# Performance work log

Measured on AMD Instinct MI355X. Metric: run time of the kernel, lower is better.

## Reference

```python
import jax, jax.numpy as jnp
import numpy as np


def setup_inputs() -> dict:
    key = jax.random.key(0)
    k1, k2 = jax.random.split(key)
    x = jax.random.normal(k1, (8, 4096, 256), dtype=jnp.float32)
    embed = jax.random.normal(k2, (1, 8192, 256), dtype=jnp.float32)
    return {"x": x, "embed": embed}


def reference(x, embed):
    # EuclideanCodebook.forward, eval mode, sample_codebook_temp=0.
    # x: [b, n, d]  (ndim < 4 -> a leading codebook dim h=1 is added)
    # embed: [h, c, d]
    xf = x.astype(jnp.float32)[None]              # [h, b, n, d]
    h, b, n, d = xf.shape
    flatten = xf.reshape(h, b * n, d)             # [h, N, d]

    # dist = -cdist(flatten, embed, p=2)
    x2 = jnp.sum(flatten * flatten, axis=-1, keepdims=True)   # [h, N, 1]
    e2 = jnp.sum(embed * embed, axis=-1)                      # [h, c]
    xe = jnp.einsum('hnd,hcd->hnc', flatten, embed)           # [h, N, c]
    d2 = jnp.maximum(x2 + e2[:, None, :] - 2.0 * xe, 0.0)
    dist = -jnp.sqrt(d2)                                      # [h, N, c]

    # gumbel_sample with temperature == 0  ->  argmax
    embed_ind = jnp.argmax(dist, axis=-1)                     # [h, N]
    embed_ind = embed_ind.reshape(h, b, n)                    # [h, b, n]

    # batched_embedding: gather codes per codebook
    quantize = jax.vmap(lambda e, i: e[i])(embed, embed_ind)  # [h, b, n, d]

    # needs_codebook_dim -> squeeze leading h
    return quantize[0], embed_ind[0]
```

## Files before the change

kernel.cpp:

```cpp
#include <hip/hip_runtime.h>
#include <math.h>

#define D       256
#define NROWS   32768
#define CODES   8192
#define QOFF    8388608

#define BM      128
#define BN      128
#define NSPL    4
#define SPLC    (CODES / NSPL)
#define NCHUNK  (SPLC / BN)
#define NSTEP   (NCHUNK * 4)
#define NBLK    1024
#define LQ      2048

#define MARG_COEF 0.016f
#define MARG_ABS  0.10f

#define OFF_AH    0ull
#define OFF_X2    16777216ull
#define OFF_NX    16908288ull
#define OFF_E2    17039360ull
#define OFF_RM    17072128ull
#define OFF_PK    17203200ull
#define OFF_MISC  17465344ull
#define OFF_BCNT  17465600ull
#define OFF_CAND  17469696ull
#define WS_NEED3  30052608ull

typedef __attribute__((ext_vector_type(8)))  short bf16x8;
typedef __attribute__((ext_vector_type(16))) float f32x16;

__device__ __forceinline__ int SWK(int b) { return b ^ (((b >> 7) & 7) << 4); }

__device__ __forceinline__ void gload16(const void* g, void* l) {
  __builtin_amdgcn_global_load_lds(
      (const __attribute__((address_space(1))) unsigned int*)g,
      (__attribute__((address_space(3))) unsigned int*)l, 16, 0, 0);
}

__device__ __forceinline__ unsigned short bf16rn(float x) {
  unsigned u = __float_as_uint(x);
  return (unsigned short)((u + 0x7fffu + ((u >> 16) & 1u)) >> 16);
}

__device__ __forceinline__ unsigned encf(float f) {
  unsigned b = __float_as_uint(f);
  return (b >> 31) ? ~b : (b | 0x80000000u);
}
__device__ __forceinline__ float decf(unsigned u) {
  return __uint_as_float((u >> 31) ? (u ^ 0x80000000u) : ~u);
}

__global__ __launch_bounds__(256) void init_kernel(unsigned* __restrict__ misc,
                                                   unsigned* __restrict__ rowMinU,
                                                   unsigned long long* __restrict__ pKey) {
  int i = blockIdx.x * 256 + threadIdx.x;
  if (i < 16) misc[i] = 0u;
  rowMinU[i] = 0xFFFFFFFFu;
  pKey[i] = ~0ull;
}

__global__ __launch_bounds__(256) void prep_kernel(const float* __restrict__ x,
                                                   const float* __restrict__ embed,
                                                   unsigned short* __restrict__ A_h,
                                                   unsigned short* __restrict__ E_h,
                                                   float* __restrict__ x2,
                                                   float* __restrict__ nx,
                                                   float* __restrict__ e2,
                                                   unsigned* __restrict__ misc) {
  int wid  = threadIdx.x >> 6;
  int lane = threadIdx.x & 63;
  int rid  = blockIdx.x * 4 + wid;
  const float* src;
  unsigned short* dst;
  if (rid < NROWS) { src = x + (size_t)rid * D;               dst = A_h + (size_t)rid * D; }
  else             { src = embed + (size_t)(rid - NROWS) * D; dst = E_h + (size_t)(rid - NROWS) * D; }
  float4 v = *(const float4*)(src + lane * 4);
  ushort4 hv = make_ushort4(bf16rn(v.x), bf16rn(v.y), bf16rn(v.z), bf16rn(v.w));
  *(ushort4*)(dst + lane * 4) = hv;
  float p = v.x * v.x + v.y * v.y + v.z * v.z + v.w * v.w;
  #pragma unroll
  for (int off = 32; off > 0; off >>= 1) p += __shfl_down(p, off);
  if (lane == 0) {
    float n = sqrtf(p);
    if (rid < NROWS) { x2[rid] = p; nx[rid] = n; }
    else { e2[rid - NROWS] = p; atomicMax(&misc[2], __float_as_uint(n)); }
  }
}

template<int MODE>
__global__ __launch_bounds__(256, 2) void gemm_pass(
    const unsigned short* __restrict__ A_h,
    const unsigned short* __restrict__ E_h,
    const float* __restrict__ e2g,
    const float* __restrict__ nxg,
    const unsigned* __restrict__ miscR,
    unsigned* __restrict__ rowMinU,
    unsigned* __restrict__ cand,
    unsigned* __restrict__ blkCnt,
    unsigned* __restrict__ ovCnt,
    unsigned OVCAP) {
  __shared__ __align__(16) char As0[16384];
  __shared__ __align__(16) char As1[16384];
  __shared__ __align__(16) char Bs0[16384];
  __shared__ __align__(16) char Bs1[16384];
  __shared__ unsigned lbuf[MODE ? LQ : 1];
  __shared__ unsigned lcnt;

  const int tid  = threadIdx.x;
  const int lane = tid & 63;
  const int wave = tid >> 6;
  const int wm = wave >> 1, wn = wave & 1;
  const int l31 = lane & 31;
  const int lh4 = (lane >> 5) << 2;
  const int rowBase = blockIdx.x * BM;
  const int split   = blockIdx.y;
  const int seg     = blockIdx.y * 256 + blockIdx.x;

  int swA[2][4], swB[2][4];
  #pragma unroll
  for (int f = 0; f < 2; f++)
    #pragma unroll
    for (int ks = 0; ks < 4; ks++) {
      int byt = ks * 32 + (lane >> 5) * 16;
      swA[f][ks] = SWK(((wm * 64 + f * 32 + l31) << 7) + byt);
      swB[f][ks] = SWK(((wn * 64 + f * 32 + l31) << 7) + byt);
    }

  int stRow[4], stCo[4], stDst[4];
  #pragma unroll
  for (int i = 0; i < 4; i++) {
    int q = i * 256 + tid;
    int u = SWK(q << 4);
    stRow[i] = u >> 7;
    stCo[i]  = u & 127;
    stDst[i] = (q & ~63) << 4;
  }

  auto STAGE = [&](char* Ad, char* Bd, int s) {
    int cc = s >> 2, kb = s & 3;
    const int cBase = split * SPLC + cc * BN;
    #pragma unroll
    for (int i = 0; i < 4; i++) {
      gload16((const char*)A_h + (((size_t)(rowBase + stRow[i])) << 9) + (kb << 7) + stCo[i],
              Ad + stDst[i]);
      gload16((const char*)E_h + (((size_t)(cBase + stRow[i])) << 9) + (kb << 7) + stCo[i],
              Bd + stDst[i]);
    }
  };

  STAGE(As0, Bs0, 0);
  if (MODE == 1 && tid == 0) lcnt = 0;

  float state[2][16];
  if (MODE == 0) {
    #pragma unroll
    for (int fm = 0; fm < 2; fm++)
      #pragma unroll
      for (int rg = 0; rg < 16; rg++) state[fm][rg] = INFINITY;
  } else {
    float neMaxF = __uint_as_float(miscR[2]);
    #pragma unroll
    for (int fm = 0; fm < 2; fm++)
      #pragma unroll
      for (int rg = 0; rg < 16; rg++) {
        int row = rowBase + wm * 64 + fm * 32 + ((rg & 3) + 8 * (rg >> 2)) + lh4;
        state[fm][rg] = decf(rowMinU[row]) + fmaf(MARG_COEF * nxg[row], neMaxF, MARG_ABS);
      }
  }

  f32x16 acc[2][2];
  #pragma unroll
  for (int i = 0; i < 2; i++)
    #pragma unroll
    for (int j = 0; j < 2; j++) acc[i][j] = (f32x16)(0.0f);

  __syncthreads();

  for (int s = 0; s < NSTEP; ++s) {
    char* Ac = (s & 1) ? As1 : As0;
    char* Bc = (s & 1) ? Bs1 : Bs0;
    if (s + 1 < NSTEP) STAGE((s & 1) ? As0 : As1, (s & 1) ? Bs0 : Bs1, s + 1);

    #pragma unroll
    for (int ks = 0; ks < 4; ++ks) {
      bf16x8 a0 = *(const bf16x8*)(Ac + swA[0][ks]);
      bf16x8 a1 = *(const bf16x8*)(Ac + swA[1][ks]);
      bf16x8 b0 = *(const bf16x8*)(Bc + swB[0][ks]);
      bf16x8 b1 = *(const bf16x8*)(Bc + swB[1][ks]);
      acc[0][0] = __builtin_amdgcn_mfma_f32_32x32x16_bf16(a0, b0, acc[0][0], 0, 0, 0);
      acc[1][0] = __builtin_amdgcn_mfma_f32_32x32x16_bf16(a1, b0, acc[1][0], 0, 0, 0);
      acc[0][1] = __builtin_amdgcn_mfma_f32_32x32x16_bf16(a0, b1, acc[0][1], 0, 0, 0);
      acc[1][1] = __builtin_amdgcn_mfma_f32_32x32x16_bf16(a1, b1, acc[1][1], 0, 0, 0);
    }

    if ((s & 3) == 3) {
      const int cc = s >> 2;
      const int cBase = split * SPLC + cc * BN;
      if (MODE == 0) {
        #pragma unroll
        for (int g = 0; g < 2; g++) {
          float e2c = e2g[cBase + wn * 64 + g * 32 + l31];
          #pragma unroll
          for (int fm = 0; fm < 2; fm++)
            #pragma unroll
            for (int rg = 0; rg < 16; rg++)
              state[fm][rg] = fminf(state[fm][rg], fmaf(acc[fm][g][rg], -2.0f, e2c));
        }
      } else {
        #pragma unroll
        for (int g = 0; g < 2; g++) {
          int col = cBase + wn * 64 + g * 32 + l31;
          float e2c = e2g[col];
          #pragma unroll
          for (int fm = 0; fm < 2; fm++)
            #pragma unroll
            for (int rg = 0; rg < 16; rg++) {
              float q = fmaf(acc[fm][g][rg], -2.0f, e2c);
              if (q <= state[fm][rg]) {
                int row = rowBase + wm * 64 + fm * 32 + ((rg & 3) + 8 * (rg >> 2)) + lh4;
                unsigned en = (unsigned)((row << 13) | col);
                unsigned p = atomicAdd(&lcnt, 1u);
                if (p < LQ) lbuf[p] = en;
                else { unsigned gp = atomicAdd(ovCnt, 1u);
                       if (gp < OVCAP) cand[(size_t)NBLK * LQ + gp] = en; }
              }
            }
        }
      }
      #pragma unroll
      for (int i = 0; i < 2; i++)
        #pragma unroll
        for (int j = 0; j < 2; j++) acc[i][j] = (f32x16)(0.0f);
    }

    __syncthreads();
  }

  if (MODE == 0) {
    #pragma unroll
    for (int fm = 0; fm < 2; fm++)
      #pragma unroll
      for (int rg = 0; rg < 16; rg++) {
        float v = state[fm][rg];
        #pragma unroll
        for (int off = 1; off < 32; off <<= 1) v = fminf(v, __shfl_xor(v, off));
        if (l31 == 0) {
          int row = rowBase + wm * 64 + fm * 32 + ((rg & 3) + 8 * (rg >> 2)) + lh4;
          atomicMin(&rowMinU[row], encf(v));
        }
      }
  } else {
    unsigned n = lcnt; if (n > LQ) n = LQ;
    for (unsigned i = tid; i < n; i += 256) cand[(size_t)seg * LQ + i] = lbuf[i];
    if (tid == 0) blkCnt[seg] = n;
  }
}

__global__ __launch_bounds__(256) void refine_kernel(const float* __restrict__ x,
                                                     const float* __restrict__ embed,
                                                     const float* __restrict__ x2g,
                                                     const float* __restrict__ e2g,
                                                     const unsigned* __restrict__ blkCnt,
                                                     const unsigned* __restrict__ cand,
                                                     const unsigned* __restrict__ miscR,
                                                     unsigned long long* __restrict__ pKey,
                                                     unsigned OVCAP) {
  const int tid = threadIdx.x;
  const int l16 = tid & 15;
  const int gid = tid >> 4;

  auto doItem = [&](unsigned pk) {
    int row = (int)(pk >> 13), col = (int)(pk & 8191u);
    double s = 0.0;
    #pragma unroll
    for (int p = 0; p < 4; p++) {
      float4 xv = *(const float4*)&x[(size_t)row * D + p * 64 + l16 * 4];
      float4 ev = *(const float4*)&embed[(size_t)col * D + p * 64 + l16 * 4];
      s = fma((double)xv.x, (double)ev.x, s);
      s = fma((double)xv.y, (double)ev.y, s);
      s = fma((double)xv.z, (double)ev.z, s);
      s = fma((double)xv.w, (double)ev.w, s);
    }
    #pragma unroll
    for (int off = 1; off < 16; off <<= 1) s += __shfl_xor(s, off);
    if (l16 == 0) {
      float xef = (float)s;
      float ss  = __fadd_rn(x2g[row], e2g[col]);
      float d2  = __fsub_rn(ss, __fmul_rn(2.0f, xef));
      d2 = fmaxf(d2, 0.0f);
      float sq = sqrtf(d2);
      unsigned long long key =
          ((unsigned long long)__float_as_uint(sq) << 32) | (unsigned)col;
      atomicMin(pKey + row, key);
    }
  };

  unsigned seg = blockIdx.x;
  unsigned n = blkCnt[seg]; if (n > LQ) n = LQ;
  const unsigned* segp = cand + (size_t)seg * LQ;
  for (unsigned i = gid; i < n; i += 16) doItem(segp[i]);

  unsigned ov = miscR[1]; if (ov > OVCAP) ov = OVCAP;
  const unsigned* ovp = cand + (size_t)NBLK * LQ;
  for (unsigned i = blockIdx.x * 16 + gid; i < ov; i += NBLK * 16) doItem(ovp[i]);
}

__global__ __launch_bounds__(256) void final_kernel(const float* __restrict__ embed,
                                                    const unsigned long long* __restrict__ pKey,
                                                    float* __restrict__ outQ,
                                                    float* __restrict__ indF) {
  int wid  = threadIdx.x >> 6;
  int lane = threadIdx.x & 63;
  int row  = blockIdx.x * 4 + wid;
  unsigned long long k = pKey[row];
  int idx = (int)(k & 8191ull);
  float4 v = *(const float4*)&embed[(size_t)idx * D + lane * 4];
  *(float4*)&outQ[(size_t)row * D + lane * 4] = v;
  if (lane == 0) indF[row] = (float)idx;
}

#define BM_F 128
#define BN_F 128
#define BK_F 32
#define NSPLIT_F 4
#define SPLIT_CF (CODES / NSPLIT_F)

__global__ __launch_bounds__(256) void sq_kernel(const float* __restrict__ x,
                                                 const float* __restrict__ embed,
                                                 float* __restrict__ x2,
                                                 float* __restrict__ e2) {
  int wid  = threadIdx.x >> 6;
  int lane = threadIdx.x & 63;
  int rid  = blockIdx.x * 4 + wid;
  const float* base = (rid < NROWS) ? (x + (size_t)rid * D)
                                    : (embed + (size_t)(rid - NROWS) * D);
  float4 v = *(const float4*)(base + lane * 4);
  float p = v.x * v.x + v.y * v.y + v.z * v.z + v.w * v.w;
  #pragma unroll
  for (int off = 32; off > 0; off >>= 1) p += __shfl_down(p, off);
  if (lane == 0) {
    if (rid < NROWS) x2[rid] = p;
    else             e2[rid - NROWS] = p;
  }
}

__global__ __launch_bounds__(256) void argmin_f32_kernel(const float* __restrict__ x,
                                                         const float* __restrict__ embed,
                                                         const float* __restrict__ x2,
                                                         const float* __restrict__ e2,
                                                         float* __restrict__ pVal,
                                                         int* __restrict__ pIdx) {
  __shared__ float As[BK_F][BM_F];
  __shared__ float Bs[BK_F][BN_F];
  const int tid = threadIdx.x;
  const int ty = tid >> 4, tx = tid & 15;
  const int rowBase = blockIdx.x * BM_F;
  const int split = blockIdx.y;
  const int r0 = ty * 8, c0 = tx * 8;
  float bestV[8]; int bestI[8];
  #pragma unroll
  for (int i = 0; i < 8; i++) { bestV[i] = -INFINITY; bestI[i] = 0; }
  float x2r[8];
  #pragma unroll
  for (int i = 0; i < 8; i++) x2r[i] = x2[rowBase + r0 + i];
  for (int chunk = 0; chunk < SPLIT_CF / BN_F; ++chunk) {
    const int cBase = split * SPLIT_CF + chunk * BN_F;
    float acc[8][8];
    #pragma unroll
    for (int i = 0; i < 8; i++)
      #pragma unroll
      for (int j = 0; j < 8; j++) acc[i][j] = 0.0f;
    for (int kb = 0; kb < D / BK_F; ++kb) {
      #pragma unroll
      for (int i = 0; i < 4; i++) {
        int f4 = tid + i * 256;
        int rr = f4 >> 3, k4 = f4 & 7;
        float4 va = *(const float4*)&x[(size_t)(rowBase + rr) * D + kb * BK_F + k4 * 4];
        As[k4 * 4 + 0][rr] = va.x; As[k4 * 4 + 1][rr] = va.y;
        As[k4 * 4 + 2][rr] = va.z; As[k4 * 4 + 3][rr] = va.w;
        float4 vb = *(const float4*)&embed[(size_t)(cBase + rr) * D + kb * BK_F + k4 * 4];
        Bs[k4 * 4 + 0][rr] = vb.x; Bs[k4 * 4 + 1][rr] = vb.y;
        Bs[k4 * 4 + 2][rr] = vb.z; Bs[k4 * 4 + 3][rr] = vb.w;
      }
      __syncthreads();
      #pragma unroll 8
      for (int kk = 0; kk < BK_F; kk++) {
        float a[8], b[8];
        *(float4*)&a[0] = *(const float4*)&As[kk][r0];
        *(float4*)&a[4] = *(const float4*)&As[kk][r0 + 4];
        *(float4*)&b[0] = *(const float4*)&Bs[kk][c0];
        *(float4*)&b[4] = *(const float4*)&Bs[kk][c0 + 4];
        #pragma unroll
        for (int i = 0; i < 8; i++)
          #pragma unroll
          for (int j = 0; j < 8; j++)
            acc[i][j] = fmaf(a[i], b[j], acc[i][j]);
      }
      __syncthreads();
    }
    #pragma unroll
    for (int j = 0; j < 8; j++) {
      int c = cBase + c0 + j;
      float e2c = e2[c];
      #pragma unroll
      for (int i = 0; i < 8; i++) {
        float s  = __fadd_rn(x2r[i], e2c);
        float u  = __fmul_rn(2.0f, acc[i][j]);
        float d2 = fmaxf(__fsub_rn(s, u), 0.0f);
        float dist = -sqrtf(d2);
        if (dist > bestV[i]) { bestV[i] = dist; bestI[i] = c; }
      }
    }
  }
  __syncthreads();
  float* Vl = &As[0][0];
  int*   Il = (int*)&Bs[0][0];
  #pragma unroll
  for (int i = 0; i < 8; i++) {
    Vl[(ty * 16 + tx) * 8 + i] = bestV[i];
    Il[(ty * 16 + tx) * 8 + i] = bestI[i];
  }
  __syncthreads();
  if (tid < BM_F) {
    int rr = tid, tyr = rr >> 3, ii = rr & 7;
    float bv = -INFINITY; int bi = 0;
    #pragma unroll
    for (int t = 0; t < 16; t++) {
      float v = Vl[(tyr * 16 + t) * 8 + ii];
      int  iv = Il[(tyr * 16 + t) * 8 + ii];
      if (v > bv || (v == bv && iv < bi)) { bv = v; bi = iv; }
    }
    pVal[split * NROWS + rowBase + rr] = bv;
    pIdx[split * NROWS + rowBase + rr] = bi;
  }
}

__global__ __launch_bounds__(256) void merge_f32_kernel(const float* __restrict__ pVal,
                                                        const int* __restrict__ pIdx,
                                                        float* __restrict__ indF) {
  int row = blockIdx.x * 256 + threadIdx.x;
  if (row >= NROWS) return;
  float bv = -INFINITY; int bi = 0;
  #pragma unroll
  for (int s = 0; s < NSPLIT_F; s++) {
    float v = pVal[s * NROWS + row];
    int  iv = pIdx[s * NROWS + row];
    if (v > bv || (v == bv && iv < bi)) { bv = v; bi = iv; }
  }
  indF[row] = (float)bi;
}

__global__ __launch_bounds__(256) void gather_f32_kernel(const float* __restrict__ embed,
                                                         const float* __restrict__ indF,
                                                         float* __restrict__ outQ) {
  int wid = threadIdx.x >> 6, lane = threadIdx.x & 63;
  int row = blockIdx.x * 4 + wid;
  int idx = (int)indF[row];
  float4 v = *(const float4*)&embed[(size_t)idx * D + lane * 4];
  *(float4*)&outQ[(size_t)row * D + lane * 4] = v;
}

extern "C" void kernel_launch(void* const* d_in, const int* in_sizes, int n_in,
                              void* d_out, int out_size, void* d_ws, size_t ws_size,
                              hipStream_t stream) {
  const float* x     = (const float*)d_in[0];
  const float* embed = (const float*)d_in[1];
  float* o = (float*)d_out;

  if (ws_size >= WS_NEED3) {
    char* w = (char*)d_ws;
    unsigned short* A_h = (unsigned short*)(w + OFF_AH);
    float* x2 = (float*)(w + OFF_X2);
    float* nx = (float*)(w + OFF_NX);
    float* e2 = (float*)(w + OFF_E2);
    unsigned* rowMinU = (unsigned*)(w + OFF_RM);
    unsigned long long* pKey = (unsigned long long*)(w + OFF_PK);
    unsigned* misc = (unsigned*)(w + OFF_MISC);
    unsigned* blkCnt = (unsigned*)(w + OFF_BCNT);
    unsigned* cand = (unsigned*)(w + OFF_CAND);
    unsigned capN  = (unsigned)((ws_size - OFF_CAND) / 4ull);
    unsigned OVCAP = capN - (unsigned)(NBLK * LQ);

    unsigned short* E_h = (unsigned short*)o;
    float* indF = o + QOFF;

    init_kernel<<<128, 256, 0, stream>>>(misc, rowMinU, pKey);
    prep_kernel<<<(NROWS + CODES) / 4, 256, 0, stream>>>(x, embed, A_h, E_h, x2, nx, e2, misc);
    dim3 gridC(NROWS / BM, NSPL);
    gemm_pass<0><<<gridC, 256, 0, stream>>>(A_h, E_h, e2, nx, misc, rowMinU,
                                            cand, blkCnt, &misc[1], OVCAP);
    gemm_pass<1><<<gridC, 256, 0, stream>>>(A_h, E_h, e2, nx, misc, rowMinU,
                                            cand, blkCnt, &misc[1], OVCAP);
    refine_kernel<<<NBLK, 256, 0, stream>>>(x, embed, x2, e2, blkCnt, cand, misc,
                                            pKey, OVCAP);
    final_kernel<<<NROWS / 4, 256, 0, stream>>>(embed, pKey, o, indF);
  } else {
    float* x2   = o;
    float* e2   = o + 32768;
    float* pVal = o + 65536;
    int*   pIdx = (int*)(o + 196608);
    float* indF = o + QOFF;
    sq_kernel<<<(NROWS + CODES) / 4, 256, 0, stream>>>(x, embed, x2, e2);
    dim3 gridB(NROWS / BM_F, NSPLIT_F);
    argmin_f32_kernel<<<gridB, 256, 0, stream>>>(x, embed, x2, e2, pVal, pIdx);
    merge_f32_kernel<<<NROWS / 256, 256, 0, stream>>>(pVal, pIdx, indF);
    gather_f32_kernel<<<NROWS / 4, 256, 0, stream>>>(embed, indF, o);
  }
}
```

Baseline: 498.4 us.

## Enlarge GEMM tiles to 256x256 with 512-thread blocks and two code splits

Both GEMM passes now compute a 256x256 output tile per block with 8 waves. Each wave holds a 64x128 sub-tile (2x4 MFMA accumulators), and the code splits drop from 4 to 2, giving 256 blocks. The LDS fragment addressing is simplified to a shared XOR offset instead of precomputed per-fragment swizzle tables. The aim is more data reuse per LDS and global load and fewer redundant row loads. In exchange, LDS use doubles to one block per CU, each block's fixed candidate queue must absorb far more candidates (more spills to the global overflow list), and the refine kernel now runs with fewer blocks.

```diff
diff --git a/kernel.cpp b/kernel.cpp
--- a/kernel.cpp
+++ b/kernel.cpp
@@ -6,13 +6,13 @@
 #define CODES   8192
 #define QOFF    8388608
 
-#define BM      128
-#define BN      128
-#define NSPL    4
+#define BM      256
+#define BN      256
+#define NSPL    2
 #define SPLC    (CODES / NSPL)
 #define NCHUNK  (SPLC / BN)
 #define NSTEP   (NCHUNK * 4)
-#define NBLK    1024
+#define NBLK    256
 #define LQ      2048
 
 #define MARG_COEF 0.016f
@@ -91,7 +91,7 @@
 }
 
 template<int MODE>
-__global__ __launch_bounds__(256, 2) void gemm_pass(
+__global__ __launch_bounds__(512, 2) void gemm_pass(
     const unsigned short* __restrict__ A_h,
     const unsigned short* __restrict__ E_h,
     const float* __restrict__ e2g,
@@ -102,37 +102,33 @@
     unsigned* __restrict__ blkCnt,
     unsigned* __restrict__ ovCnt,
     unsigned OVCAP) {
-  __shared__ __align__(16) char As0[16384];
-  __shared__ __align__(16) char As1[16384];
-  __shared__ __align__(16) char Bs0[16384];
-  __shared__ __align__(16) char Bs1[16384];
+  __shared__ __align__(16) char As0[32768];
+  __shared__ __align__(16) char As1[32768];
+  __shared__ __align__(16) char Bs0[32768];
+  __shared__ __align__(16) char Bs1[32768];
   __shared__ unsigned lbuf[MODE ? LQ : 1];
   __shared__ unsigned lcnt;
 
   const int tid  = threadIdx.x;
   const int lane = tid & 63;
   const int wave = tid >> 6;
-  const int wm = wave >> 1, wn = wave & 1;
+  const int wm = wave >> 1;
+  const int wn = wave & 1;
   const int l31 = lane & 31;
-  const int lh4 = (lane >> 5) << 2;
+  const int hi16 = (lane >> 5) << 4;
+  const int lh4  = (lane >> 5) << 2;
   const int rowBase = blockIdx.x * BM;
   const int split   = blockIdx.y;
-  const int seg     = blockIdx.y * 256 + blockIdx.x;
-
-  int swA[2][4], swB[2][4];
-  #pragma unroll
-  for (int f = 0; f < 2; f++)
-    #pragma unroll
-    for (int ks = 0; ks < 4; ks++) {
-      int byt = ks * 32 + (lane >> 5) * 16;
-      swA[f][ks] = SWK(((wm * 64 + f * 32 + l31) << 7) + byt);
-      swB[f][ks] = SWK(((wn * 64 + f * 32 + l31) << 7) + byt);
-    }
+  const int seg     = blockIdx.y * 128 + blockIdx.x;
+
+  const int Ccom = hi16 ^ ((l31 & 7) << 4);
+  const int Aoff = (wm * 64 + l31) << 7;
+  const int Boff = (wn * 128 + l31) << 7;
 
   int stRow[4], stCo[4], stDst[4];
   #pragma unroll
   for (int i = 0; i < 4; i++) {
-    int q = i * 256 + tid;
+    int q = i * 512 + tid;
     int u = SWK(q << 4);
     stRow[i] = u >> 7;
     stCo[i]  = u & 127;
@@ -171,11 +167,11 @@
       }
   }
 
-  f32x16 acc[2][2];
+  f32x16 acc[2][4];
   #pragma unroll
   for (int i = 0; i < 2; i++)
     #pragma unroll
-    for (int j = 0; j < 2; j++) acc[i][j] = (f32x16)(0.0f);
+    for (int j = 0; j < 4; j++) acc[i][j] = (f32x16)(0.0f);
 
   __syncthreads();
 
@@ -186,14 +182,21 @@
 
     #pragma unroll
     for (int ks = 0; ks < 4; ++ks) {
-      bf16x8 a0 = *(const bf16x8*)(Ac + swA[0][ks]);
-      bf16x8 a1 = *(const bf16x8*)(Ac + swA[1][ks]);
-      bf16x8 b0 = *(const bf16x8*)(Bc + swB[0][ks]);
-      bf16x8 b1 = *(const bf16x8*)(Bc + swB[1][ks]);
+      const int off = Ccom ^ (ks << 5);
+      bf16x8 a0 = *(const bf16x8*)(Ac + Aoff + off);
+      bf16x8 a1 = *(const bf16x8*)(Ac + Aoff + 4096 + off);
+      bf16x8 b0 = *(const bf16x8*)(Bc + Boff + off);
+      bf16x8 b1 = *(const bf16x8*)(Bc + Boff + 4096 + off);
+      bf16x8 b2 = *(const bf16x8*)(Bc + Boff + 8192 + off);
+      bf16x8 b3 = *(const bf16x8*)(Bc + Boff + 12288 + off);
       acc[0][0] = __builtin_amdgcn_mfma_f32_32x32x16_bf16(a0, b0, acc[0][0], 0, 0, 0);
       acc[1][0] = __builtin_amdgcn_mfma_f32_32x32x16_bf16(a1, b0, acc[1][0], 0, 0, 0);
       acc[0][1] = __builtin_amdgcn_mfma_f32_32x32x16_bf16(a0, b1, acc[0][1], 0, 0, 0);
       acc[1][1] = __builtin_amdgcn_mfma_f32_32x32x16_bf16(a1, b1, acc[1][1], 0, 0, 0);
+      acc[0][2] = __builtin_amdgcn_mfma_f32_32x32x16_bf16(a0, b2, acc[0][2], 0, 0, 0);
+      acc[1][2] = __builtin_amdgcn_mfma_f32_32x32x16_bf16(a1, b2, acc[1][2], 0, 0, 0);
+      acc[0][3] = __builtin_amdgcn_mfma_f32_32x32x16_bf16(a0, b3, acc[0][3], 0, 0, 0);
+      acc[1][3] = __builtin_amdgcn_mfma_f32_32x32x16_bf16(a1, b3, acc[1][3], 0, 0, 0);
     }
 
     if ((s & 3) == 3) {
@@ -201,8 +204,8 @@
       const int cBase = split * SPLC + cc * BN;
       if (MODE == 0) {
         #pragma unroll
-        for (int g = 0; g < 2; g++) {
-          float e2c = e2g[cBase + wn * 64 + g * 32 + l31];
+        for (int g = 0; g < 4; g++) {
+          float e2c = e2g[cBase + wn * 128 + g * 32 + l31];
           #pragma unroll
           for (int fm = 0; fm < 2; fm++)
             #pragma unroll
@@ -211,8 +214,8 @@
         }
       } else {
         #pragma unroll
-        for (int g = 0; g < 2; g++) {
-          int col = cBase + wn * 64 + g * 32 + l31;
+        for (int g = 0; g < 4; g++) {
+          int col = cBase + wn * 128 + g * 32 + l31;
           float e2c = e2g[col];
           #pragma unroll
           for (int fm = 0; fm < 2; fm++)
@@ -233,7 +236,7 @@
       #pragma unroll
       for (int i = 0; i < 2; i++)
         #pragma unroll
-        for (int j = 0; j < 2; j++) acc[i][j] = (f32x16)(0.0f);
+        for (int j = 0; j < 4; j++) acc[i][j] = (f32x16)(0.0f);
     }
 
     __syncthreads();
@@ -254,7 +257,7 @@
       }
   } else {
     unsigned n = lcnt; if (n > LQ) n = LQ;
-    for (unsigned i = tid; i < n; i += 256) cand[(size_t)seg * LQ + i] = lbuf[i];
+    for (unsigned i = tid; i < n; i += 512) cand[(size_t)seg * LQ + i] = lbuf[i];
     if (tid == 0) blkCnt[seg] = n;
   }
 }
@@ -490,9 +493,9 @@
     init_kernel<<<128, 256, 0, stream>>>(misc, rowMinU, pKey);
     prep_kernel<<<(NROWS + CODES) / 4, 256, 0, stream>>>(x, embed, A_h, E_h, x2, nx, e2, misc);
     dim3 gridC(NROWS / BM, NSPL);
-    gemm_pass<0><<<gridC, 256, 0, stream>>>(A_h, E_h, e2, nx, misc, rowMinU,
+    gemm_pass<0><<<gridC, 512, 0, stream>>>(A_h, E_h, e2, nx, misc, rowMinU,
                                             cand, blkCnt, &misc[1], OVCAP);
-    gemm_pass<1><<<gridC, 256, 0, stream>>>(A_h, E_h, e2, nx, misc, rowMinU,
+    gemm_pass<1><<<gridC, 512, 0, stream>>>(A_h, E_h, e2, nx, misc, rowMinU,
                                             cand, blkCnt, &misc[1], OVCAP);
     refine_kernel<<<NBLK, 256, 0, stream>>>(x, embed, x2, e2, blkCnt, cand, misc,
                                             pKey, OVCAP);
```

Result: faster. 444.4 us (-10.8%).

## Keep A tile in registers, drop code split, stream B through 4-slot ring

Applied to the files above, without the earlier changes.

The GEMM passes no longer split the codebook across four grid columns. Each block now covers all 8192 codes for its 128 rows, keeps its A fragments resident in registers, and streams only E tiles through a 4-deep LDS ring with explicit vmcnt waits. The e2 vector is preloaded into LDS, and MFMA sections raise wave priority. This removes repeated A staging and the per-split block overhead, but the grid shrinks to 256 blocks at one block per CU, which lowers occupancy and may underfill the GPU.

```diff
diff --git a/kernel.cpp b/kernel.cpp
--- a/kernel.cpp
+++ b/kernel.cpp
@@ -8,11 +8,9 @@
 
 #define BM      128
 #define BN      128
-#define NSPL    4
-#define SPLC    (CODES / NSPL)
-#define NCHUNK  (SPLC / BN)
+#define NCHUNK  (CODES / BN)
 #define NSTEP   (NCHUNK * 4)
-#define NBLK    1024
+#define NBLK    256
 #define LQ      2048
 
 #define MARG_COEF 0.016f
@@ -91,7 +89,7 @@
 }
 
 template<int MODE>
-__global__ __launch_bounds__(256, 2) void gemm_pass(
+__global__ __launch_bounds__(256, 1) void gemm_pass(
     const unsigned short* __restrict__ A_h,
     const unsigned short* __restrict__ E_h,
     const float* __restrict__ e2g,
@@ -102,32 +100,24 @@
     unsigned* __restrict__ blkCnt,
     unsigned* __restrict__ ovCnt,
     unsigned OVCAP) {
-  __shared__ __align__(16) char As0[16384];
-  __shared__ __align__(16) char As1[16384];
-  __shared__ __align__(16) char Bs0[16384];
-  __shared__ __align__(16) char Bs1[16384];
+  __shared__ __align__(16) char ring[4][16384];
+  __shared__ __align__(16) float e2s[CODES];
   __shared__ unsigned lbuf[MODE ? LQ : 1];
   __shared__ unsigned lcnt;
 
   const int tid  = threadIdx.x;
   const int lane = tid & 63;
   const int wave = tid >> 6;
-  const int wm = wave >> 1, wn = wave & 1;
+  const int wm = wave >> 1;
+  const int wn = wave & 1;
   const int l31 = lane & 31;
-  const int lh4 = (lane >> 5) << 2;
+  const int hi16 = (lane >> 5) << 4;
+  const int lh4  = (lane >> 5) << 2;
   const int rowBase = blockIdx.x * BM;
-  const int split   = blockIdx.y;
-  const int seg     = blockIdx.y * 256 + blockIdx.x;
-
-  int swA[2][4], swB[2][4];
-  #pragma unroll
-  for (int f = 0; f < 2; f++)
-    #pragma unroll
-    for (int ks = 0; ks < 4; ks++) {
-      int byt = ks * 32 + (lane >> 5) * 16;
-      swA[f][ks] = SWK(((wm * 64 + f * 32 + l31) << 7) + byt);
-      swB[f][ks] = SWK(((wn * 64 + f * 32 + l31) << 7) + byt);
-    }
+  const int seg     = blockIdx.x;
+
+  const int Ccom = hi16 ^ ((l31 & 7) << 4);
+  const int Boff = (wn * 64 + l31) << 7;
 
   int stRow[4], stCo[4], stDst[4];
   #pragma unroll
@@ -139,21 +129,6 @@
     stDst[i] = (q & ~63) << 4;
   }
 
-  auto STAGE = [&](char* Ad, char* Bd, int s) {
-    int cc = s >> 2, kb = s & 3;
-    const int cBase = split * SPLC + cc * BN;
-    #pragma unroll
-    for (int i = 0; i < 4; i++) {
-      gload16((const char*)A_h + (((size_t)(rowBase + stRow[i])) << 9) + (kb << 7) + stCo[i],
-              Ad + stDst[i]);
-      gload16((const char*)E_h + (((size_t)(cBase + stRow[i])) << 9) + (kb << 7) + stCo[i],
-              Bd + stDst[i]);
-    }
-  };
-
-  STAGE(As0, Bs0, 0);
-  if (MODE == 1 && tid == 0) lcnt = 0;
-
   float state[2][16];
   if (MODE == 0) {
     #pragma unroll
@@ -171,72 +146,111 @@
       }
   }
 
+  bf16x8 af[2][16];
+  #pragma unroll
+  for (int fm = 0; fm < 2; fm++) {
+    const char* ab = (const char*)A_h
+        + (((size_t)(rowBase + wm * 64 + fm * 32 + l31)) << 9) + hi16;
+    #pragma unroll
+    for (int k = 0; k < 16; k++)
+      af[fm][k] = *(const bf16x8*)(ab + k * 32);
+  }
+  asm volatile("s_waitcnt vmcnt(0)" ::: "memory");
+  if (MODE == 1 && tid == 0) lcnt = 0;
+
+  auto STAGE = [&](int slot, int s) {
+    const int cBase = (s >> 2) * BN;
+    const int kb = s & 3;
+    #pragma unroll
+    for (int i = 0; i < 4; i++)
+      gload16((const char*)E_h + (((size_t)(cBase + stRow[i])) << 9) + (kb << 7) + stCo[i],
+              ring[slot] + stDst[i]);
+  };
+
+  #pragma unroll
+  for (int j = 0; j < 8; j++) {
+    int q2 = j * 256 + tid;
+    gload16((const char*)e2g + (size_t)q2 * 16, (char*)e2s + ((q2 & ~63) << 4));
+  }
+  STAGE(0, 0); STAGE(1, 1); STAGE(2, 2);
+
   f32x16 acc[2][2];
   #pragma unroll
   for (int i = 0; i < 2; i++)
     #pragma unroll
     for (int j = 0; j < 2; j++) acc[i][j] = (f32x16)(0.0f);
 
-  __syncthreads();
-
-  for (int s = 0; s < NSTEP; ++s) {
-    char* Ac = (s & 1) ? As1 : As0;
-    char* Bc = (s & 1) ? Bs1 : Bs0;
-    if (s + 1 < NSTEP) STAGE((s & 1) ? As0 : As1, (s & 1) ? Bs0 : Bs1, s + 1);
-
-    #pragma unroll
-    for (int ks = 0; ks < 4; ++ks) {
-      bf16x8 a0 = *(const bf16x8*)(Ac + swA[0][ks]);
-      bf16x8 a1 = *(const bf16x8*)(Ac + swA[1][ks]);
-      bf16x8 b0 = *(const bf16x8*)(Bc + swB[0][ks]);
-      bf16x8 b1 = *(const bf16x8*)(Bc + swB[1][ks]);
-      acc[0][0] = __builtin_amdgcn_mfma_f32_32x32x16_bf16(a0, b0, acc[0][0], 0, 0, 0);
-      acc[1][0] = __builtin_amdgcn_mfma_f32_32x32x16_bf16(a1, b0, acc[1][0], 0, 0, 0);
-      acc[0][1] = __builtin_amdgcn_mfma_f32_32x32x16_bf16(a0, b1, acc[0][1], 0, 0, 0);
-      acc[1][1] = __builtin_amdgcn_mfma_f32_32x32x16_bf16(a1, b1, acc[1][1], 0, 0, 0);
+  for (int cc = 0; cc < NCHUNK; ++cc) {
+    #pragma unroll
+    for (int kb = 0; kb < 4; ++kb) {
+      const int s = cc * 4 + kb;
+      if (s + 3 < NSTEP) {
+        STAGE((kb + 3) & 3, s + 3);
+        asm volatile("s_waitcnt vmcnt(12)" ::: "memory");
+      } else if (s + 2 < NSTEP) {
+        asm volatile("s_waitcnt vmcnt(8)" ::: "memory");
+      } else if (s + 1 < NSTEP) {
+        asm volatile("s_waitcnt vmcnt(4)" ::: "memory");
+      } else {
+        asm volatile("s_waitcnt vmcnt(0)" ::: "memory");
+      }
+      asm volatile("s_barrier" ::: "memory");
+
+      const char* Bc = ring[kb];
+      __builtin_amdgcn_s_setprio(1);
+      #pragma unroll
+      for (int ks = 0; ks < 4; ++ks) {
+        const int off = Ccom ^ (ks << 5);
+        bf16x8 b0 = *(const bf16x8*)(Bc + Boff + off);
+        bf16x8 b1 = *(const bf16x8*)(Bc + Boff + 4096 + off);
+        acc[0][0] = __builtin_amdgcn_mfma_f32_32x32x16_bf16(af[0][kb * 4 + ks], b0, acc[0][0], 0, 0, 0);
+        acc[1][0] = __builtin_amdgcn_mfma_f32_32x32x16_bf16(af[1][kb * 4 + ks], b0, acc[1][0], 0, 0, 0);
+        acc[0][1] = __builtin_amdgcn_mfma_f32_32x32x16_bf16(af[0][kb * 4 + ks], b1, acc[0][1], 0, 0, 0);
+        acc[1][1] = __builtin_amdgcn_mfma_f32_32x32x16_bf16(af[1][kb * 4 + ks], b1, acc[1][1], 0, 0, 0);
+      }
+      __builtin_amdgcn_s_setprio(0);
+
+      if (kb == 3) {
+        const int cBase = cc * BN;
+        if (MODE == 0) {
+          #pragma unroll
+          for (int g = 0; g < 2; g++) {
+            float e2c = e2s[cBase + wn * 64 + g * 32 + l31];
+            #pragma unroll
+            for (int fm = 0; fm < 2; fm++)
+              #pragma unroll
+              for (int rg = 0; rg < 16; rg++)
+                state[fm][rg] = fminf(state[fm][rg], fmaf(acc[fm][g][rg], -2.0f, e2c));
+          }
+        } else {
+          #pragma unroll
+          for (int g = 0; g < 2; g++) {
+            int col = cBase + wn * 64 + g * 32 + l31;
+            float e2c = e2s[col];
+            #pragma unroll
+            for (int fm = 0; fm < 2; fm++)
+              #pragma unroll
+              for (int rg = 0; rg < 16; rg++) {
+                float q = fmaf(acc[fm][g][rg], -2.0f, e2c);
+                if (q <= state[fm][rg]) {
+                  int row = rowBase + wm * 64 + fm * 32 + ((rg & 3) + 8 * (rg >> 2)) + lh4;
+                  unsigned en = (unsigned)((row << 13) | col);
+                  unsigned p = atomicAdd(&lcnt, 1u);
+                  if (p < LQ) lbuf[p] = en;
+                  else { unsigned gp = atomicAdd(ovCnt, 1u);
+                         if (gp < OVCAP) cand[(size_t)NBLK * LQ + gp] = en; }
+                }
+              }
+          }
+        }
+        #pragma unroll
+        for (int i = 0; i < 2; i++)
+          #pragma unroll
+          for (int j = 0; j < 2; j++) acc[i][j] = (f32x16)(0.0f);
+      }
+
+      asm volatile("s_waitcnt lgkmcnt(0)\n\ts_barrier" ::: "memory");
     }
-
-    if ((s & 3) == 3) {
-      const int cc = s >> 2;
-      const int cBase = split * SPLC + cc * BN;
-      if (MODE == 0) {
-        #pragma unroll
-        for (int g = 0; g < 2; g++) {
-          float e2c = e2g[cBase + wn * 64 + g * 32 + l31];
-          #pragma unroll
-          for (int fm = 0; fm < 2; fm++)
-            #pragma unroll
-            for (int rg = 0; rg < 16; rg++)
-              state[fm][rg] = fminf(state[fm][rg], fmaf(acc[fm][g][rg], -2.0f, e2c));
-        }
-      } else {
-        #pragma unroll
-        for (int g = 0; g < 2; g++) {
-          int col = cBase + wn * 64 + g * 32 + l31;
-          float e2c = e2g[col];
-          #pragma unroll
-          for (int fm = 0; fm < 2; fm++)
-            #pragma unroll
-            for (int rg = 0; rg < 16; rg++) {
-              float q = fmaf(acc[fm][g][rg], -2.0f, e2c);
-              if (q <= state[fm][rg]) {
-                int row = rowBase + wm * 64 + fm * 32 + ((rg & 3) + 8 * (rg >> 2)) + lh4;
-                unsigned en = (unsigned)((row << 13) | col);
-                unsigned p = atomicAdd(&lcnt, 1u);
-                if (p < LQ) lbuf[p] = en;
-                else { unsigned gp = atomicAdd(ovCnt, 1u);
-                       if (gp < OVCAP) cand[(size_t)NBLK * LQ + gp] = en; }
-              }
-            }
-        }
-      }
-      #pragma unroll
-      for (int i = 0; i < 2; i++)
-        #pragma unroll
-        for (int j = 0; j < 2; j++) acc[i][j] = (f32x16)(0.0f);
-    }
-
-    __syncthreads();
   }
 
   if (MODE == 0) {
@@ -253,6 +267,7 @@
         }
       }
   } else {
+    __syncthreads();
     unsigned n = lcnt; if (n > LQ) n = LQ;
     for (unsigned i = tid; i < n; i += 256) cand[(size_t)seg * LQ + i] = lbuf[i];
     if (tid == 0) blkCnt[seg] = n;
@@ -489,11 +504,10 @@
 
     init_kernel<<<128, 256, 0, stream>>>(misc, rowMinU, pKey);
     prep_kernel<<<(NROWS + CODES) / 4, 256, 0, stream>>>(x, embed, A_h, E_h, x2, nx, e2, misc);
-    dim3 gridC(NROWS / BM, NSPL);
-    gemm_pass<0><<<gridC, 256, 0, stream>>>(A_h, E_h, e2, nx, misc, rowMinU,
-                                            cand, blkCnt, &misc[1], OVCAP);
-    gemm_pass<1><<<gridC, 256, 0, stream>>>(A_h, E_h, e2, nx, misc, rowMinU,
-                                            cand, blkCnt, &misc[1], OVCAP);
+    gemm_pass<0><<<NBLK, 256, 0, stream>>>(A_h, E_h, e2, nx, misc, rowMinU,
+                                           cand, blkCnt, &misc[1], OVCAP);
+    gemm_pass<1><<<NBLK, 256, 0, stream>>>(A_h, E_h, e2, nx, misc, rowMinU,
+                                           cand, blkCnt, &misc[1], OVCAP);
     refine_kernel<<<NBLK, 256, 0, stream>>>(x, embed, x2, e2, blkCnt, cand, misc,
                                             pKey, OVCAP);
     final_kernel<<<NROWS / 4, 256, 0, stream>>>(embed, pKey, o, indF);
```

Result: slower. 551.0 us (+10.6%).
